# Kernel tuning notes

Hardware: AMD Instinct MI355X
Metric: run time of the kernel (lower is better)

The kernel has to match this reference:

```python
import jax, jax.numpy as jnp
import numpy as np

ALPHA_LEAKY = 0.2
EPS = 1e-10


def setup_inputs() -> dict:
    key = jax.random.key(0)
    k1, k2, k3, k4 = jax.random.split(key, 4)
    N, E, IN_DIM, OUT_DIM = 50000, 800000, 128, 64
    node_features = jax.random.normal(k1, (N, IN_DIM), dtype=jnp.float32)
    edge_index = jax.random.randint(k2, (2, E), 0, N, dtype=jnp.int64)
    # xavier_uniform with gain=1.414
    def xavier(k, shape, gain=1.414):
        fan_in, fan_out = shape[1], shape[0]
        bound = gain * np.sqrt(6.0 / (fan_in + fan_out))
        return jax.random.uniform(k, shape, jnp.float32, -bound, bound)
    W = xavier(k3, (OUT_DIM, IN_DIM))          # nn.Linear weight layout [out, in]
    a = xavier(k4, (1, 2 * OUT_DIM))           # attention vector [1, 2*out]
    return {"node_features": node_features, "edge_index": edge_index, "W": W, "a": a}


def reference(node_features, edge_index, W, a):
    # h = W(node_features): [N, out_dim]
    h = node_features @ W.T
    num_nodes, out_dim = h.shape
    src = edge_index[0]
    tgt = edge_index[1]
    # a @ cat([h_src, h_tgt]) decomposes into per-node partial scores (no [E, 2d] concat)
    s_src = h @ a[0, :out_dim]   # [N]
    s_tgt = h @ a[0, out_dim:]   # [N]
    e = jax.nn.leaky_relu(s_src[src] + s_tgt[tgt], negative_slope=ALPHA_LEAKY)  # [E]
    # segment softmax over incoming edges of each target node
    e_max = jax.ops.segment_max(e, tgt, num_segments=num_nodes)
    e_exp = jnp.exp(e - e_max[tgt])
    e_sum = jax.ops.segment_sum(e_exp, tgt, num_segments=num_nodes)
    attention = e_exp / (e_sum[tgt] + EPS)
    # weighted scatter-add aggregation of source features into targets
    h_prime = jax.ops.segment_sum(h[src] * attention[:, None], tgt, num_segments=num_nodes)
    return jax.nn.elu(h_prime)
```

## Files before the change

### kernel.cpp

```cpp
#include <hip/hip_runtime.h>
#include <math.h>

#define ALPHA_LEAKY 0.2f
#define EPS_F 1e-10f
#define NBMAX 1024
#define NBLK 128

typedef __attribute__((ext_vector_type(8))) short short8;
typedef __attribute__((ext_vector_type(4))) float f32x4;

__device__ __forceinline__ unsigned short bf16_rne(float f) {
    unsigned u = __float_as_uint(f);
    u += 0x7FFFu + ((u >> 16) & 1u);
    return (unsigned short)(u >> 16);
}

__global__ void k_prep(const float* __restrict__ W, uint4* __restrict__ Wbf) {
    int f = blockIdx.x * 256 + threadIdx.x;
    int nt = f >> 8;
    if (nt >= 4) return;
    int l = f & 63, kt = (f >> 6) & 3;
    int nn = nt * 16 + (l & 15);
    int k  = kt * 32 + (l >> 4) * 8;
    const float* wr = W + nn * 128 + k;
    unsigned short b[8];
    #pragma unroll
    for (int j = 0; j < 8; ++j) b[j] = bf16_rne(wr[j]);
    uint4 v;
    v.x = (unsigned)b[0] | ((unsigned)b[1] << 16);
    v.y = (unsigned)b[2] | ((unsigned)b[3] << 16);
    v.z = (unsigned)b[4] | ((unsigned)b[5] << 16);
    v.w = (unsigned)b[6] | ((unsigned)b[7] << 16);
    Wbf[f] = v;
}

__global__ __launch_bounds__(256) void k_gemm(
    const float* __restrict__ X, const uint4* __restrict__ Wbf,
    const float* __restrict__ a, unsigned short* __restrict__ hb,
    float* __restrict__ s_src, float* __restrict__ s_tgt, int n, int nstripes) {
    const int lane = threadIdx.x & 63;
    const int ml = lane & 15, g = lane >> 4;
    short8 bfr[4][4];
    #pragma unroll
    for (int nt = 0; nt < 4; ++nt)
        #pragma unroll
        for (int kt = 0; kt < 4; ++kt) {
            uint4 v = Wbf[(nt * 4 + kt) * 64 + lane];
            bfr[nt][kt] = *(short8*)&v;
        }
    float as[4], at[4];
    #pragma unroll
    for (int nt = 0; nt < 4; ++nt) {
        as[nt] = a[nt * 16 + ml];
        at[nt] = a[64 + nt * 16 + ml];
    }
    for (int stripe = blockIdx.x * 4 + (threadIdx.x >> 6); stripe < nstripes;
         stripe += gridDim.x * 4) {
        const int row0 = stripe * 16;
        const int rrow = min(row0 + ml, n - 1);
        const float* xr = X + (size_t)rrow * 128;
        f32x4 acc[4] = {{0.f,0.f,0.f,0.f},{0.f,0.f,0.f,0.f},
                        {0.f,0.f,0.f,0.f},{0.f,0.f,0.f,0.f}};
        #pragma unroll
        for (int kt = 0; kt < 4; ++kt) {
            float4 x0 = *(const float4*)(xr + kt * 32 + g * 8);
            float4 x1 = *(const float4*)(xr + kt * 32 + g * 8 + 4);
            short8 af;
            af[0] = (short)bf16_rne(x0.x); af[1] = (short)bf16_rne(x0.y);
            af[2] = (short)bf16_rne(x0.z); af[3] = (short)bf16_rne(x0.w);
            af[4] = (short)bf16_rne(x1.x); af[5] = (short)bf16_rne(x1.y);
            af[6] = (short)bf16_rne(x1.z); af[7] = (short)bf16_rne(x1.w);
            #pragma unroll
            for (int nt = 0; nt < 4; ++nt)
                acc[nt] = __builtin_amdgcn_mfma_f32_16x16x32_bf16(
                    af, bfr[nt][kt], acc[nt], 0, 0, 0);
        }
        #pragma unroll
        for (int reg = 0; reg < 4; ++reg) {
            int row = row0 + g * 4 + reg;
            float p = acc[0][reg] * as[0] + acc[1][reg] * as[1] +
                      acc[2][reg] * as[2] + acc[3][reg] * as[3];
            float q = acc[0][reg] * at[0] + acc[1][reg] * at[1] +
                      acc[2][reg] * at[2] + acc[3][reg] * at[3];
            #pragma unroll
            for (int off = 1; off < 16; off <<= 1) {
                p += __shfl_xor(p, off, 64);
                q += __shfl_xor(q, off, 64);
            }
            if (ml == 0 && row < n) { s_src[row] = p; s_tgt[row] = q; }
        }
        #pragma unroll
        for (int nt = 0; nt < 4; ++nt)
            #pragma unroll
            for (int reg = 0; reg < 4; ++reg) {
                int row = row0 + g * 4 + reg;
                if (row < n)
                    hb[(size_t)row * 64 + nt * 16 + ml] = bf16_rne(acc[nt][reg]);
            }
    }
}

__global__ __launch_bounds__(256) void k_hist(
    const int* __restrict__ ei, int* __restrict__ histg, int nb, int E, int epb) {
    __shared__ int hist[NBMAX];
    const int t = threadIdx.x;
    for (int k = t; k < nb; k += 256) hist[k] = 0;
    __syncthreads();
    const int e0 = blockIdx.x * epb, e1 = min(e0 + epb, E);
    for (int e = e0 + t; e < e1; e += 256)
        atomicAdd(&hist[ei[E + e] >> 6], 1);
    __syncthreads();
    int* outp = histg + (size_t)blockIdx.x * nb;
    for (int k = t; k < nb; k += 256) outp[k] = hist[k];
}

__global__ __launch_bounds__(256) void k_colscan(
    int* __restrict__ histg, int* __restrict__ btot, int nb) {
    __shared__ int wsum[4];
    const int bucket = blockIdx.x;
    const int t = threadIdx.x, lane = t & 63, w = t >> 6;
    int v = (t < NBLK) ? histg[(size_t)t * nb + bucket] : 0;
    int pre = v;
    #pragma unroll
    for (int off = 1; off < 64; off <<= 1) {
        int x = __shfl_up(pre, off, 64);
        if (lane >= off) pre += x;
    }
    if (lane == 63) wsum[w] = pre;
    __syncthreads();
    int wb = 0;
    for (int k = 0; k < w; ++k) wb += wsum[k];
    if (t < NBLK) histg[(size_t)t * nb + bucket] = wb + pre - v;
    if (t == 255) btot[bucket] = wsum[0] + wsum[1] + wsum[2] + wsum[3];
}

__global__ __launch_bounds__(256) void k_bscan(
    const int* __restrict__ btot, int* __restrict__ bstart, int nb, int E) {
    __shared__ int wsum[4];
    int t = threadIdx.x;
    int lane = t & 63, w = t >> 6;
    int v[4]; int sum = 0;
    #pragma unroll
    for (int j = 0; j < 4; ++j) {
        int idx = t * 4 + j;
        v[j] = (idx < nb) ? btot[idx] : 0;
        sum += v[j];
    }
    int pre = sum;
    #pragma unroll
    for (int off = 1; off < 64; off <<= 1) {
        int x = __shfl_up(pre, off, 64);
        if (lane >= off) pre += x;
    }
    if (lane == 63) wsum[w] = pre;
    __syncthreads();
    int wbase = 0;
    for (int k = 0; k < w; ++k) wbase += wsum[k];
    int run = wbase + pre - sum;
    #pragma unroll
    for (int j = 0; j < 4; ++j) {
        int idx = t * 4 + j;
        if (idx < nb) bstart[idx] = run;
        run += v[j];
    }
    if (t == 255) bstart[nb] = E;
}

__global__ __launch_bounds__(256) void k_place(
    const int* __restrict__ ei, const int* __restrict__ histg,
    const int* __restrict__ bstart, unsigned* __restrict__ st,
    int nb, int E, int epb) {
    __shared__ int cur[NBMAX];
    const int t = threadIdx.x;
    const int* my = histg + (size_t)blockIdx.x * nb;
    for (int k = t; k < nb; k += 256) cur[k] = bstart[k] + my[k];
    __syncthreads();
    const int e0 = blockIdx.x * epb, e1 = min(e0 + epb, E);
    for (int e = e0 + t; e < e1; e += 256) {
        int s  = ei[e];
        int tt = ei[E + e];
        int slot = atomicAdd(&cur[tt >> 6], 1);
        st[slot] = ((unsigned)s << 6) | (unsigned)(tt & 63);
    }
}

__global__ __launch_bounds__(256) void k_local(
    const unsigned* __restrict__ st, const int* __restrict__ bstart,
    int* __restrict__ base, int* __restrict__ deg, int* __restrict__ csr_src,
    int n) {
    __shared__ int hist[64];
    __shared__ int nbase[64];
    const int b = blockIdx.x;
    const int n0 = b << 6;
    const int t = threadIdx.x;
    if (t < 64) hist[t] = 0;
    __syncthreads();
    const int s0 = bstart[b], s1 = bstart[b + 1];
    for (int i = s0 + t; i < s1; i += 256)
        atomicAdd(&hist[st[i] & 63u], 1);
    __syncthreads();
    if (t < 64) {
        int v = hist[t];
        int pre = v;
        #pragma unroll
        for (int off = 1; off < 64; off <<= 1) {
            int x = __shfl_up(pre, off, 64);
            if (t >= off) pre += x;
        }
        int bs = s0 + pre - v;
        nbase[t] = bs;
        if (n0 + t < n) { base[n0 + t] = bs; deg[n0 + t] = v; }
    }
    __syncthreads();
    if (t < 64) hist[t] = nbase[t];
    __syncthreads();
    for (int i = s0 + t; i < s1; i += 256) {
        unsigned p = st[i];
        int slot = atomicAdd(&hist[p & 63u], 1);
        csr_src[slot] = (int)(p >> 6);
    }
}

__device__ __forceinline__ void accum8(float acc[8], uint4 hv, float w) {
    unsigned u[4] = {hv.x, hv.y, hv.z, hv.w};
    #pragma unroll
    for (int i = 0; i < 4; ++i) {
        float lo = __uint_as_float(u[i] << 16);
        float hi = __uint_as_float(u[i] & 0xFFFF0000u);
        acc[2 * i]     = fmaf(w, lo, acc[2 * i]);
        acc[2 * i + 1] = fmaf(w, hi, acc[2 * i + 1]);
    }
}

__global__ __launch_bounds__(256) void k_node(
    const int* __restrict__ base, const int* __restrict__ deg,
    const int* __restrict__ csr_src, const float* __restrict__ s_src,
    const float* __restrict__ s_tgt, const unsigned short* __restrict__ hb,
    float* __restrict__ out, int n) {
    const int lane = threadIdx.x & 63;
    const int node = blockIdx.x * 4 + (threadIdx.x >> 6);
    if (node >= n) return;
    const int b = base[node];
    const int d = deg[node];
    const float st = s_tgt[node];
    const int g = lane >> 3, r = lane & 7;
    float acc[8] = {0.f, 0.f, 0.f, 0.f, 0.f, 0.f, 0.f, 0.f};

    if (d <= 64) {
        int src_l = 0; float w_l = 0.f, v = -INFINITY;
        if (lane < d) {
            src_l = csr_src[b + lane];
            float x = s_src[src_l] + st;
            v = (x > 0.f) ? x : ALPHA_LEAKY * x;
        }
        float m = v;
        #pragma unroll
        for (int off = 32; off > 0; off >>= 1) m = fmaxf(m, __shfl_xor(m, off, 64));
        float ex = (lane < d) ? expf(v - m) : 0.f;
        float sum = ex;
        #pragma unroll
        for (int off = 32; off > 0; off >>= 1) sum += __shfl_xor(sum, off, 64);
        w_l = ex * (1.f / (sum + EPS_F));
        for (int k = 0; k < d; k += 8) {
            int ke = k + g;
            int s   = __shfl(src_l, ke, 64);
            float w = __shfl(w_l,  ke, 64);
            uint4 hv = ((const uint4*)(hb + (size_t)s * 64))[r];
            accum8(acc, hv, w);
        }
    } else {
        float m = -INFINITY;
        for (int c = lane; c < d; c += 64) {
            float x = s_src[csr_src[b + c]] + st;
            x = (x > 0.f) ? x : ALPHA_LEAKY * x;
            m = fmaxf(m, x);
        }
        #pragma unroll
        for (int off = 32; off > 0; off >>= 1) m = fmaxf(m, __shfl_xor(m, off, 64));
        float sum = 0.f;
        for (int c = lane; c < d; c += 64) {
            float x = s_src[csr_src[b + c]] + st;
            x = (x > 0.f) ? x : ALPHA_LEAKY * x;
            sum += expf(x - m);
        }
        #pragma unroll
        for (int off = 32; off > 0; off >>= 1) sum += __shfl_xor(sum, off, 64);
        float inv = 1.f / (sum + EPS_F);
        for (int c0 = 0; c0 < d; c0 += 64) {
            int j = c0 + lane;
            int src_l = 0; float w_l = 0.f;
            if (j < d) {
                src_l = csr_src[b + j];
                float x = s_src[src_l] + st;
                x = (x > 0.f) ? x : ALPHA_LEAKY * x;
                w_l = expf(x - m) * inv;
            }
            int lim = min(64, d - c0);
            for (int k = 0; k < lim; k += 8) {
                int ke = k + g;
                int s   = __shfl(src_l, ke, 64);
                float w = __shfl(w_l,  ke, 64);
                uint4 hv = ((const uint4*)(hb + (size_t)s * 64))[r];
                accum8(acc, hv, w);
            }
        }
    }

    #pragma unroll
    for (int off = 8; off <= 32; off <<= 1) {
        #pragma unroll
        for (int j = 0; j < 8; ++j) acc[j] += __shfl_xor(acc[j], off, 64);
    }
    if (g == 0) {
        float4 o0, o1;
        o0.x = acc[0] > 0.f ? acc[0] : expf(acc[0]) - 1.f;
        o0.y = acc[1] > 0.f ? acc[1] : expf(acc[1]) - 1.f;
        o0.z = acc[2] > 0.f ? acc[2] : expf(acc[2]) - 1.f;
        o0.w = acc[3] > 0.f ? acc[3] : expf(acc[3]) - 1.f;
        o1.x = acc[4] > 0.f ? acc[4] : expf(acc[4]) - 1.f;
        o1.y = acc[5] > 0.f ? acc[5] : expf(acc[5]) - 1.f;
        o1.z = acc[6] > 0.f ? acc[6] : expf(acc[6]) - 1.f;
        o1.w = acc[7] > 0.f ? acc[7] : expf(acc[7]) - 1.f;
        float4* o4 = (float4*)out + (size_t)node * 16;
        o4[r * 2]     = o0;
        o4[r * 2 + 1] = o1;
    }
}

extern "C" void kernel_launch(void* const* d_in, const int* in_sizes, int n_in,
                              void* d_out, int out_size, void* d_ws, size_t ws_size,
                              hipStream_t stream) {
    const float* X  = (const float*)d_in[0];
    const int*   ei = (const int*)d_in[1];
    const float* W  = (const float*)d_in[2];
    const float* a  = (const float*)d_in[3];
    float* out = (float*)d_out;

    const int N = in_sizes[0] / 128;
    const int E = in_sizes[1] / 2;
    const int nb = (N + 63) >> 6;
    const int epb = (E + NBLK - 1) / NBLK;

    char* p = (char*)d_ws;
    unsigned short* hb = (unsigned short*)p; p += (size_t)N * 64 * sizeof(unsigned short);
    uint4*    Wbf    = (uint4*)p;    p += 1024 * sizeof(uint4);
    float*    s_src  = (float*)p;    p += (size_t)N * sizeof(float);
    float*    s_tgt  = (float*)p;    p += (size_t)N * sizeof(float);
    int*      deg    = (int*)p;      p += (size_t)N * sizeof(int);
    int*      base   = (int*)p;      p += (size_t)N * sizeof(int);
    int*      histg  = (int*)p;      p += (size_t)NBLK * nb * sizeof(int);
    int*      btot   = (int*)p;      p += (size_t)nb * sizeof(int);
    int*      bstart = (int*)p;      p += (size_t)(nb + 1) * sizeof(int);
    int*      csr_src= (int*)p;      p += (size_t)E * sizeof(int);
    unsigned* st     = (unsigned*)p;

    const int nstripes = (N + 15) / 16;
    k_prep   <<<4, 256, 0, stream>>>(W, Wbf);
    k_gemm   <<<(nstripes + 3) / 4, 256, 0, stream>>>(X, Wbf, a, hb, s_src, s_tgt, N, nstripes);
    k_hist   <<<NBLK, 256, 0, stream>>>(ei, histg, nb, E, epb);
    k_colscan<<<nb, 256, 0, stream>>>(histg, btot, nb);
    k_bscan  <<<1, 256, 0, stream>>>(btot, bstart, nb, E);
    k_place  <<<NBLK, 256, 0, stream>>>(ei, histg, bstart, st, nb, E, epb);
    k_local  <<<nb, 256, 0, stream>>>(st, bstart, base, deg, csr_src, N);
    k_node   <<<(N + 3) / 4, 256, 0, stream>>>(base, deg, csr_src, s_src, s_tgt, hb, out, N);
}
```

Baseline: 151.0 us.

## Fuse bucket-local CSR build into the node aggregation kernel via LDS

Drops the separate k_local pass and its global csr_src/base/deg arrays. Each 64-node bucket block now sorts its edges into shared memory and then runs the softmax and aggregation for its 16-node-per-wave slice directly. Buckets larger than CAP fall back to rescanning the whole segment per node. Also doubles NBLK for the histogram and place passes so k_colscan uses all 256 threads. The fused kernel launches far fewer blocks, about 782 with 16 nodes per wave processed serially, and uses 16 KB of LDS, which may lower occupancy and latency hiding for the gathers.

```diff
diff --git a/kernel.cpp b/kernel.cpp
--- a/kernel.cpp
+++ b/kernel.cpp
@@ -4,7 +4,8 @@
 #define ALPHA_LEAKY 0.2f
 #define EPS_F 1e-10f
 #define NBMAX 1024
-#define NBLK 128
+#define NBLK 256
+#define CAP  4096
 
 typedef __attribute__((ext_vector_type(8))) short short8;
 typedef __attribute__((ext_vector_type(4))) float f32x4;
@@ -119,7 +120,7 @@
     __shared__ int wsum[4];
     const int bucket = blockIdx.x;
     const int t = threadIdx.x, lane = t & 63, w = t >> 6;
-    int v = (t < NBLK) ? histg[(size_t)t * nb + bucket] : 0;
+    int v = histg[(size_t)t * nb + bucket];
     int pre = v;
     #pragma unroll
     for (int off = 1; off < 64; off <<= 1) {
@@ -130,8 +131,8 @@
     __syncthreads();
     int wb = 0;
     for (int k = 0; k < w; ++k) wb += wsum[k];
-    if (t < NBLK) histg[(size_t)t * nb + bucket] = wb + pre - v;
-    if (t == 255) btot[bucket] = wsum[0] + wsum[1] + wsum[2] + wsum[3];
+    histg[(size_t)t * nb + bucket] = wb + pre - v;
+    if (t == 255) btot[bucket] = wb + pre;
 }
 
 __global__ __launch_bounds__(256) void k_bscan(
@@ -184,43 +185,6 @@
     }
 }
 
-__global__ __launch_bounds__(256) void k_local(
-    const unsigned* __restrict__ st, const int* __restrict__ bstart,
-    int* __restrict__ base, int* __restrict__ deg, int* __restrict__ csr_src,
-    int n) {
-    __shared__ int hist[64];
-    __shared__ int nbase[64];
-    const int b = blockIdx.x;
-    const int n0 = b << 6;
-    const int t = threadIdx.x;
-    if (t < 64) hist[t] = 0;
-    __syncthreads();
-    const int s0 = bstart[b], s1 = bstart[b + 1];
-    for (int i = s0 + t; i < s1; i += 256)
-        atomicAdd(&hist[st[i] & 63u], 1);
-    __syncthreads();
-    if (t < 64) {
-        int v = hist[t];
-        int pre = v;
-        #pragma unroll
-        for (int off = 1; off < 64; off <<= 1) {
-            int x = __shfl_up(pre, off, 64);
-            if (t >= off) pre += x;
-        }
-        int bs = s0 + pre - v;
-        nbase[t] = bs;
-        if (n0 + t < n) { base[n0 + t] = bs; deg[n0 + t] = v; }
-    }
-    __syncthreads();
-    if (t < 64) hist[t] = nbase[t];
-    __syncthreads();
-    for (int i = s0 + t; i < s1; i += 256) {
-        unsigned p = st[i];
-        int slot = atomicAdd(&hist[p & 63u], 1);
-        csr_src[slot] = (int)(p >> 6);
-    }
-}
-
 __device__ __forceinline__ void accum8(float acc[8], uint4 hv, float w) {
     unsigned u[4] = {hv.x, hv.y, hv.z, hv.w};
     #pragma unroll
@@ -232,98 +196,222 @@
     }
 }
 
-__global__ __launch_bounds__(256) void k_node(
-    const int* __restrict__ base, const int* __restrict__ deg,
-    const int* __restrict__ csr_src, const float* __restrict__ s_src,
-    const float* __restrict__ s_tgt, const unsigned short* __restrict__ hb,
-    float* __restrict__ out, int n) {
-    const int lane = threadIdx.x & 63;
-    const int node = blockIdx.x * 4 + (threadIdx.x >> 6);
-    if (node >= n) return;
-    const int b = base[node];
-    const int d = deg[node];
-    const float st = s_tgt[node];
+__global__ __launch_bounds__(256) void k_bnode2(
+    const unsigned* __restrict__ st, const int* __restrict__ bstart,
+    const float* __restrict__ s_src, const float* __restrict__ s_tgt,
+    const unsigned short* __restrict__ hb, float* __restrict__ out, int n) {
+    __shared__ int st_lds[CAP];
+    __shared__ int hist[64];
+    __shared__ int base_lds[64];
+    __shared__ int deg_lds[64];
+    __shared__ int cur[64];
+    __shared__ float stgt_lds[64];
+    const int b = blockIdx.x;
+    const int n0 = b << 6;
+    const int t = threadIdx.x;
+    const int lane = t & 63;
+    const int w = t >> 6;
     const int g = lane >> 3, r = lane & 7;
-    float acc[8] = {0.f, 0.f, 0.f, 0.f, 0.f, 0.f, 0.f, 0.f};
-
-    if (d <= 64) {
-        int src_l = 0; float w_l = 0.f, v = -INFINITY;
-        if (lane < d) {
-            src_l = csr_src[b + lane];
-            float x = s_src[src_l] + st;
-            v = (x > 0.f) ? x : ALPHA_LEAKY * x;
-        }
-        float m = v;
-        #pragma unroll
-        for (int off = 32; off > 0; off >>= 1) m = fmaxf(m, __shfl_xor(m, off, 64));
-        float ex = (lane < d) ? expf(v - m) : 0.f;
-        float sum = ex;
-        #pragma unroll
-        for (int off = 32; off > 0; off >>= 1) sum += __shfl_xor(sum, off, 64);
-        w_l = ex * (1.f / (sum + EPS_F));
-        for (int k = 0; k < d; k += 8) {
-            int ke = k + g;
-            int s   = __shfl(src_l, ke, 64);
-            float w = __shfl(w_l,  ke, 64);
-            uint4 hv = ((const uint4*)(hb + (size_t)s * 64))[r];
-            accum8(acc, hv, w);
+    const int s0 = bstart[b], seg = bstart[b + 1] - s0;
+
+    if (t < 64) {
+        hist[t] = 0;
+        int node = n0 + t;
+        stgt_lds[t] = (node < n) ? s_tgt[node] : 0.f;
+    }
+    __syncthreads();
+
+    if (seg <= CAP) {
+        unsigned mine[16];
+        #pragma unroll
+        for (int j = 0; j < 16; ++j) {
+            int i = t + j * 256;
+            mine[j] = 0xFFFFFFFFu;
+            if (i < seg) {
+                unsigned p = st[s0 + i];
+                mine[j] = p;
+                atomicAdd(&hist[p & 63u], 1);
+            }
+        }
+        __syncthreads();
+        if (t < 64) {
+            int v = hist[t];
+            int pre = v;
+            #pragma unroll
+            for (int off = 1; off < 64; off <<= 1) {
+                int x = __shfl_up(pre, off, 64);
+                if (t >= off) pre += x;
+            }
+            int bs = pre - v;
+            base_lds[t] = bs;
+            deg_lds[t] = v;
+            cur[t] = bs;
+        }
+        __syncthreads();
+        #pragma unroll
+        for (int j = 0; j < 16; ++j) {
+            if (mine[j] != 0xFFFFFFFFu) {
+                int slot = atomicAdd(&cur[mine[j] & 63u], 1);
+                st_lds[slot] = (int)(mine[j] >> 6);
+            }
+        }
+        __syncthreads();
+
+        for (int nl = w * 16; nl < w * 16 + 16; ++nl) {
+            const int node = n0 + nl;
+            const int bb = base_lds[nl];
+            const int d = deg_lds[nl];
+            const float stg = stgt_lds[nl];
+            float acc[8] = {0.f,0.f,0.f,0.f,0.f,0.f,0.f,0.f};
+            if (d <= 64) {
+                int src_l = 0; float v = -INFINITY;
+                if (lane < d) {
+                    src_l = st_lds[bb + lane];
+                    float x = s_src[src_l] + stg;
+                    v = (x > 0.f) ? x : ALPHA_LEAKY * x;
+                }
+                float m = v;
+                #pragma unroll
+                for (int off = 32; off > 0; off >>= 1) m = fmaxf(m, __shfl_xor(m, off, 64));
+                float ex = (lane < d) ? expf(v - m) : 0.f;
+                float sum = ex;
+                #pragma unroll
+                for (int off = 32; off > 0; off >>= 1) sum += __shfl_xor(sum, off, 64);
+                float w_l = ex * (1.f / (sum + EPS_F));
+                for (int k = 0; k < d; k += 8) {
+                    int ke = k + g;
+                    int s    = __shfl(src_l, ke, 64);
+                    float wv = __shfl(w_l,  ke, 64);
+                    uint4 hv = ((const uint4*)(hb + (size_t)s * 64))[r];
+                    accum8(acc, hv, wv);
+                }
+            } else {
+                float m = -INFINITY;
+                for (int c = lane; c < d; c += 64) {
+                    float x = s_src[st_lds[bb + c]] + stg;
+                    x = (x > 0.f) ? x : ALPHA_LEAKY * x;
+                    m = fmaxf(m, x);
+                }
+                #pragma unroll
+                for (int off = 32; off > 0; off >>= 1) m = fmaxf(m, __shfl_xor(m, off, 64));
+                float sum = 0.f;
+                for (int c = lane; c < d; c += 64) {
+                    float x = s_src[st_lds[bb + c]] + stg;
+                    x = (x > 0.f) ? x : ALPHA_LEAKY * x;
+                    sum += expf(x - m);
+                }
+                #pragma unroll
+                for (int off = 32; off > 0; off >>= 1) sum += __shfl_xor(sum, off, 64);
+                float inv = 1.f / (sum + EPS_F);
+                for (int c0 = 0; c0 < d; c0 += 64) {
+                    int j = c0 + lane;
+                    int src_l = 0; float w_l = 0.f;
+                    if (j < d) {
+                        src_l = st_lds[bb + j];
+                        float x = s_src[src_l] + stg;
+                        x = (x > 0.f) ? x : ALPHA_LEAKY * x;
+                        w_l = expf(x - m) * inv;
+                    }
+                    int lim = min(64, d - c0);
+                    for (int k = 0; k < lim; k += 8) {
+                        int ke = k + g;
+                        int s    = __shfl(src_l, ke, 64);
+                        float wv = __shfl(w_l,  ke, 64);
+                        uint4 hv = ((const uint4*)(hb + (size_t)s * 64))[r];
+                        accum8(acc, hv, wv);
+                    }
+                }
+            }
+            #pragma unroll
+            for (int off = 8; off <= 32; off <<= 1) {
+                #pragma unroll
+                for (int j = 0; j < 8; ++j) acc[j] += __shfl_xor(acc[j], off, 64);
+            }
+            if (g == 0 && node < n) {
+                float4 o0, o1;
+                o0.x = acc[0] > 0.f ? acc[0] : expf(acc[0]) - 1.f;
+                o0.y = acc[1] > 0.f ? acc[1] : expf(acc[1]) - 1.f;
+                o0.z = acc[2] > 0.f ? acc[2] : expf(acc[2]) - 1.f;
+                o0.w = acc[3] > 0.f ? acc[3] : expf(acc[3]) - 1.f;
+                o1.x = acc[4] > 0.f ? acc[4] : expf(acc[4]) - 1.f;
+                o1.y = acc[5] > 0.f ? acc[5] : expf(acc[5]) - 1.f;
+                o1.z = acc[6] > 0.f ? acc[6] : expf(acc[6]) - 1.f;
+                o1.w = acc[7] > 0.f ? acc[7] : expf(acc[7]) - 1.f;
+                float4* o4 = (float4*)out + (size_t)node * 16;
+                o4[r * 2]     = o0;
+                o4[r * 2 + 1] = o1;
+            }
         }
     } else {
-        float m = -INFINITY;
-        for (int c = lane; c < d; c += 64) {
-            float x = s_src[csr_src[b + c]] + st;
-            x = (x > 0.f) ? x : ALPHA_LEAKY * x;
-            m = fmaxf(m, x);
-        }
-        #pragma unroll
-        for (int off = 32; off > 0; off >>= 1) m = fmaxf(m, __shfl_xor(m, off, 64));
-        float sum = 0.f;
-        for (int c = lane; c < d; c += 64) {
-            float x = s_src[csr_src[b + c]] + st;
-            x = (x > 0.f) ? x : ALPHA_LEAKY * x;
-            sum += expf(x - m);
-        }
-        #pragma unroll
-        for (int off = 32; off > 0; off >>= 1) sum += __shfl_xor(sum, off, 64);
-        float inv = 1.f / (sum + EPS_F);
-        for (int c0 = 0; c0 < d; c0 += 64) {
-            int j = c0 + lane;
-            int src_l = 0; float w_l = 0.f;
-            if (j < d) {
-                src_l = csr_src[b + j];
-                float x = s_src[src_l] + st;
-                x = (x > 0.f) ? x : ALPHA_LEAKY * x;
-                w_l = expf(x - m) * inv;
-            }
-            int lim = min(64, d - c0);
-            for (int k = 0; k < lim; k += 8) {
-                int ke = k + g;
-                int s   = __shfl(src_l, ke, 64);
-                float w = __shfl(w_l,  ke, 64);
-                uint4 hv = ((const uint4*)(hb + (size_t)s * 64))[r];
-                accum8(acc, hv, w);
-            }
-        }
-    }
-
-    #pragma unroll
-    for (int off = 8; off <= 32; off <<= 1) {
-        #pragma unroll
-        for (int j = 0; j < 8; ++j) acc[j] += __shfl_xor(acc[j], off, 64);
-    }
-    if (g == 0) {
-        float4 o0, o1;
-        o0.x = acc[0] > 0.f ? acc[0] : expf(acc[0]) - 1.f;
-        o0.y = acc[1] > 0.f ? acc[1] : expf(acc[1]) - 1.f;
-        o0.z = acc[2] > 0.f ? acc[2] : expf(acc[2]) - 1.f;
-        o0.w = acc[3] > 0.f ? acc[3] : expf(acc[3]) - 1.f;
-        o1.x = acc[4] > 0.f ? acc[4] : expf(acc[4]) - 1.f;
-        o1.y = acc[5] > 0.f ? acc[5] : expf(acc[5]) - 1.f;
-        o1.z = acc[6] > 0.f ? acc[6] : expf(acc[6]) - 1.f;
-        o1.w = acc[7] > 0.f ? acc[7] : expf(acc[7]) - 1.f;
-        float4* o4 = (float4*)out + (size_t)node * 16;
-        o4[r * 2]     = o0;
-        o4[r * 2 + 1] = o1;
+        for (int nl = w * 16; nl < w * 16 + 16; ++nl) {
+            const int node = n0 + nl;
+            if (node >= n) continue;
+            const float stg = stgt_lds[nl];
+            float m = -INFINITY;
+            for (int c = lane; c < seg; c += 64) {
+                unsigned p = st[s0 + c];
+                if ((int)(p & 63u) == nl) {
+                    float x = s_src[p >> 6] + stg;
+                    x = (x > 0.f) ? x : ALPHA_LEAKY * x;
+                    m = fmaxf(m, x);
+                }
+            }
+            #pragma unroll
+            for (int off = 32; off > 0; off >>= 1) m = fmaxf(m, __shfl_xor(m, off, 64));
+            float sum = 0.f;
+            for (int c = lane; c < seg; c += 64) {
+                unsigned p = st[s0 + c];
+                if ((int)(p & 63u) == nl) {
+                    float x = s_src[p >> 6] + stg;
+                    x = (x > 0.f) ? x : ALPHA_LEAKY * x;
+                    sum += expf(x - m);
+                }
+            }
+            #pragma unroll
+            for (int off = 32; off > 0; off >>= 1) sum += __shfl_xor(sum, off, 64);
+            float inv = 1.f / (sum + EPS_F);
+            float acc[8] = {0.f,0.f,0.f,0.f,0.f,0.f,0.f,0.f};
+            for (int c0 = 0; c0 < seg; c0 += 64) {
+                int j = c0 + lane;
+                int src_l = 0; float w_l = 0.f;
+                if (j < seg) {
+                    unsigned p = st[s0 + j];
+                    if ((int)(p & 63u) == nl) {
+                        src_l = p >> 6;
+                        float x = s_src[src_l] + stg;
+                        x = (x > 0.f) ? x : ALPHA_LEAKY * x;
+                        w_l = expf(x - m) * inv;
+                    }
+                }
+                int lim = min(64, seg - c0);
+                for (int k = 0; k < lim; k += 8) {
+                    int ke = k + g;
+                    int s    = __shfl(src_l, ke, 64);
+                    float wv = __shfl(w_l,  ke, 64);
+                    uint4 hv = ((const uint4*)(hb + (size_t)s * 64))[r];
+                    accum8(acc, hv, wv);
+                }
+            }
+            #pragma unroll
+            for (int off = 8; off <= 32; off <<= 1) {
+                #pragma unroll
+                for (int j = 0; j < 8; ++j) acc[j] += __shfl_xor(acc[j], off, 64);
+            }
+            if (g == 0) {
+                float4 o0, o1;
+                o0.x = acc[0] > 0.f ? acc[0] : expf(acc[0]) - 1.f;
+                o0.y = acc[1] > 0.f ? acc[1] : expf(acc[1]) - 1.f;
+                o0.z = acc[2] > 0.f ? acc[2] : expf(acc[2]) - 1.f;
+                o0.w = acc[3] > 0.f ? acc[3] : expf(acc[3]) - 1.f;
+                o1.x = acc[4] > 0.f ? acc[4] : expf(acc[4]) - 1.f;
+                o1.y = acc[5] > 0.f ? acc[5] : expf(acc[5]) - 1.f;
+                o1.z = acc[6] > 0.f ? acc[6] : expf(acc[6]) - 1.f;
+                o1.w = acc[7] > 0.f ? acc[7] : expf(acc[7]) - 1.f;
+                float4* o4 = (float4*)out + (size_t)node * 16;
+                o4[r * 2]     = o0;
+                o4[r * 2 + 1] = o1;
+            }
+        }
     }
 }
 
@@ -346,12 +434,9 @@
     uint4*    Wbf    = (uint4*)p;    p += 1024 * sizeof(uint4);
     float*    s_src  = (float*)p;    p += (size_t)N * sizeof(float);
     float*    s_tgt  = (float*)p;    p += (size_t)N * sizeof(float);
-    int*      deg    = (int*)p;      p += (size_t)N * sizeof(int);
-    int*      base   = (int*)p;      p += (size_t)N * sizeof(int);
     int*      histg  = (int*)p;      p += (size_t)NBLK * nb * sizeof(int);
     int*      btot   = (int*)p;      p += (size_t)nb * sizeof(int);
     int*      bstart = (int*)p;      p += (size_t)(nb + 1) * sizeof(int);
-    int*      csr_src= (int*)p;      p += (size_t)E * sizeof(int);
     unsigned* st     = (unsigned*)p;
 
     const int nstripes = (N + 15) / 16;
@@ -361,6 +446,5 @@
     k_colscan<<<nb, 256, 0, stream>>>(histg, btot, nb);
     k_bscan  <<<1, 256, 0, stream>>>(btot, bstart, nb, E);
     k_place  <<<NBLK, 256, 0, stream>>>(ei, histg, bstart, st, nb, E, epb);
-    k_local  <<<nb, 256, 0, stream>>>(st, bstart, base, deg, csr_src, N);
-    k_node   <<<(N + 3) / 4, 256, 0, stream>>>(base, deg, csr_src, s_src, s_tgt, hb, out, N);
-}
+    k_bnode2 <<<nb, 256, 0, stream>>>(st, bstart, s_src, s_tgt, hb, out, N);
+}
```

New measurement: 158.3 us. 4.8% more time.
